# Optimization experiments

Measured on AMD Instinct MI355X. Metric: run time of the kernel, lower is better.

## Reference

```python
import jax, jax.numpy as jnp
import numpy as np


def setup_inputs() -> dict:
    key = jax.random.key(0)
    k1, k2 = jax.random.split(key)
    B, H, W, C = 8, 256, 256, 64
    image = jax.random.normal(k1, (B, H, W, C), dtype=jnp.float32)
    flow = jax.random.normal(k2, (B, H, W, 2), dtype=jnp.float32)
    return {"image": image, "flow": flow}


def dense_image_warp(image, flow):
    """Faithful port of tfa.image.dense_image_warp.

    query_points = grid(y,x) - flow, then bilinear interpolation with
    floor indices clamped to [0, size-2] and alphas clipped to [0, 1]
    (matching tfa's interpolate_bilinear with indexing='ij').
    """
    B, H, W, C = image.shape
    gy, gx = jnp.meshgrid(jnp.arange(H, dtype=flow.dtype),
                          jnp.arange(W, dtype=flow.dtype), indexing="ij")
    qy = gy[None] - flow[..., 0]  # [B,H,W]
    qx = gx[None] - flow[..., 1]  # [B,H,W]

    fy = jnp.clip(jnp.floor(qy), 0.0, H - 2)
    fx = jnp.clip(jnp.floor(qx), 0.0, W - 2)
    ay = jnp.clip(qy - fy, 0.0, 1.0)[..., None]  # [B,H,W,1]
    ax = jnp.clip(qx - fx, 0.0, 1.0)[..., None]

    iy = fy.astype(jnp.int32)
    ix = fx.astype(jnp.int32)
    b = jnp.arange(B)[:, None, None]

    tl = image[b, iy, ix]          # [B,H,W,C]
    tr = image[b, iy, ix + 1]
    bl = image[b, iy + 1, ix]
    br = image[b, iy + 1, ix + 1]

    top = tl + ax * (tr - tl)
    bot = bl + ax * (br - bl)
    return top + ay * (bot - top)


def reference(image, flow):
    return dense_image_warp(image, flow)
```

## Files before the change

### kernel.cpp

```cpp
#include <hip/hip_runtime.h>


__global__ __launch_bounds__(256) void warp_bilinear_kernel(
    const float* __restrict__ image,
    const float* __restrict__ flow,
    float* __restrict__ out)
{
    constexpr int H = 256, W = 256, C = 64;
    constexpr int QUADS = C / 4;

    const int gid = blockIdx.x * blockDim.x + threadIdx.x;
    const int p = gid >> 4;
    const int q = gid & 15;

    const int x = p & (W - 1);
    const int y = (p >> 8) & (H - 1);
    const int b = p >> 16;

    const float qy = (float)y - flow[2 * p + 0];
    const float qx = (float)x - flow[2 * p + 1];

    const float fy = fminf(fmaxf(floorf(qy), 0.0f), (float)(H - 2));
    const float fx = fminf(fmaxf(floorf(qx), 0.0f), (float)(W - 2));
    const float ay = fminf(fmaxf(qy - fy, 0.0f), 1.0f);
    const float ax = fminf(fmaxf(qx - fx, 0.0f), 1.0f);
    const int iy = (int)fy;
    const int ix = (int)fx;

    const float4* __restrict__ img4 = (const float4*)image;
    const long base = (((long)(b * H + iy)) * W + ix) * QUADS + q;
    const long rowstep = (long)W * QUADS;

    const float4 tl = img4[base];
    const float4 tr = img4[base + QUADS];
    const float4 bl = img4[base + rowstep];
    const float4 br = img4[base + rowstep + QUADS];

    float4 r;
    {
        float top, bot;
        top = fmaf(ax, tr.x - tl.x, tl.x);
        bot = fmaf(ax, br.x - bl.x, bl.x);
        r.x = fmaf(ay, bot - top, top);
        top = fmaf(ax, tr.y - tl.y, tl.y);
        bot = fmaf(ax, br.y - bl.y, bl.y);
        r.y = fmaf(ay, bot - top, top);
        top = fmaf(ax, tr.z - tl.z, tl.z);
        bot = fmaf(ax, br.z - bl.z, bl.z);
        r.z = fmaf(ay, bot - top, top);
        top = fmaf(ax, tr.w - tl.w, tl.w);
        bot = fmaf(ax, br.w - bl.w, bl.w);
        r.w = fmaf(ay, bot - top, top);
    }

    ((float4*)out)[gid] = r;
}

extern "C" void kernel_launch(void* const* d_in, const int* in_sizes, int n_in,
                              void* d_out, int out_size, void* d_ws, size_t ws_size,
                              hipStream_t stream) {
    const float* image = (const float*)d_in[0];
    const float* flow  = (const float*)d_in[1];
    float* out = (float*)d_out;

    constexpr int B = 8, H = 256, W = 256, C = 64;
    const int total_threads = B * H * W * (C / 4);
    const int block = 256;
    const int grid = total_threads / block;

    warp_bilinear_kernel<<<grid, block, 0, stream>>>(image, flow, out);
}
```

Baseline: 229.0 us.

## Process two channel quads per thread with nontemporal output stores

```diff
diff --git a/kernel.cpp b/kernel.cpp
--- a/kernel.cpp
+++ b/kernel.cpp
@@ -1,5 +1,7 @@
 #include <hip/hip_runtime.h>
 
+
+typedef float f4 __attribute__((ext_vector_type(4)));
 
 __global__ __launch_bounds__(256) void warp_bilinear_kernel(
     const float* __restrict__ image,
@@ -8,17 +10,18 @@
 {
     constexpr int H = 256, W = 256, C = 64;
     constexpr int QUADS = C / 4;
+    constexpr int R = W * QUADS;
 
     const int gid = blockIdx.x * blockDim.x + threadIdx.x;
-    const int p = gid >> 4;
-    const int q = gid & 15;
+    const int p = gid >> 3;
+    const int q = gid & 7;
 
     const int x = p & (W - 1);
     const int y = (p >> 8) & (H - 1);
-    const int b = p >> 16;
 
-    const float qy = (float)y - flow[2 * p + 0];
-    const float qx = (float)x - flow[2 * p + 1];
+    const float2 fl = ((const float2*)flow)[p];
+    const float qy = (float)y - fl.x;
+    const float qx = (float)x - fl.y;
 
     const float fy = fminf(fmaxf(floorf(qy), 0.0f), (float)(H - 2));
     const float fx = fminf(fmaxf(floorf(qx), 0.0f), (float)(W - 2));
@@ -27,33 +30,34 @@
     const int iy = (int)fy;
     const int ix = (int)fx;
 
-    const float4* __restrict__ img4 = (const float4*)image;
-    const long base = (((long)(b * H + iy)) * W + ix) * QUADS + q;
-    const long rowstep = (long)W * QUADS;
+    const f4* __restrict__ img4 = (const f4*)image;
+    const int base = ((p & ~0xFFFF) + (iy << 8) + ix) * QUADS + q;
 
-    const float4 tl = img4[base];
-    const float4 tr = img4[base + QUADS];
-    const float4 bl = img4[base + rowstep];
-    const float4 br = img4[base + rowstep + QUADS];
+    const f4 tl0 = img4[base];
+    const f4 tr0 = img4[base + QUADS];
+    const f4 bl0 = img4[base + R];
+    const f4 br0 = img4[base + R + QUADS];
+    const f4 tl1 = img4[base + 8];
+    const f4 tr1 = img4[base + QUADS + 8];
+    const f4 bl1 = img4[base + R + 8];
+    const f4 br1 = img4[base + R + QUADS + 8];
 
-    float4 r;
-    {
+    f4 r0, r1;
+    #pragma unroll
+    for (int e = 0; e < 4; ++e) {
         float top, bot;
-        top = fmaf(ax, tr.x - tl.x, tl.x);
-        bot = fmaf(ax, br.x - bl.x, bl.x);
-        r.x = fmaf(ay, bot - top, top);
-        top = fmaf(ax, tr.y - tl.y, tl.y);
-        bot = fmaf(ax, br.y - bl.y, bl.y);
-        r.y = fmaf(ay, bot - top, top);
-        top = fmaf(ax, tr.z - tl.z, tl.z);
-        bot = fmaf(ax, br.z - bl.z, bl.z);
-        r.z = fmaf(ay, bot - top, top);
-        top = fmaf(ax, tr.w - tl.w, tl.w);
-        bot = fmaf(ax, br.w - bl.w, bl.w);
-        r.w = fmaf(ay, bot - top, top);
+        top = fmaf(ax, tr0[e] - tl0[e], tl0[e]);
+        bot = fmaf(ax, br0[e] - bl0[e], bl0[e]);
+        r0[e] = fmaf(ay, bot - top, top);
+        top = fmaf(ax, tr1[e] - tl1[e], tl1[e]);
+        bot = fmaf(ax, br1[e] - bl1[e], bl1[e]);
+        r1[e] = fmaf(ay, bot - top, top);
     }
 
-    ((float4*)out)[gid] = r;
+    f4* o4 = (f4*)out;
+    const int oidx = p * QUADS + q;
+    __builtin_nontemporal_store(r0, o4 + oidx);
+    __builtin_nontemporal_store(r1, o4 + oidx + 8);
 }
 
 extern "C" void kernel_launch(void* const* d_in, const int* in_sizes, int n_in,
@@ -63,8 +67,8 @@
     const float* flow  = (const float*)d_in[1];
     float* out = (float*)d_out;
 
-    constexpr int B = 8, H = 256, W = 256, C = 64;
-    const int total_threads = B * H * W * (C / 4);
+    constexpr int B = 8, H = 256, W = 256;
+    const int total_threads = B * H * W * 8;
     const int block = 256;
     const int grid = total_threads / block;
 
```

Measured after the change: 231.1 us. No clear change (+0.9%).
